# Kernel optimization log

Measured on AMD Instinct MI355X. Metric: run time of the kernel, lower is better.

Reference implementation:

```python
import jax, jax.numpy as jnp
import numpy as np


def setup_inputs() -> dict:
    key = jax.random.key(0)
    k1, k2, k3 = jax.random.split(key, 3)
    B, S, N = 32, 128, 256
    input_real = jax.random.normal(k1, (B, S, N), dtype=jnp.float32)
    input_imag = jax.random.normal(k2, (B, S, N), dtype=jnp.float32)
    weight = jax.random.uniform(k3, (B, S), dtype=jnp.float32)
    return {"input_real": input_real, "input_imag": input_imag, "weight": weight}


def reference(input_real, input_imag, weight):
    # Weighted mixture of rank-1 density matrices over the sequence dim S.
    # output_real[b,n,m] = sum_s w[b,s] * (r[b,s,n]*r[b,s,m] + i[b,s,n]*i[b,s,m])
    # output_imag[b,n,m] = sum_s w[b,s] * (i[b,s,n]*r[b,s,m] - r[b,s,n]*i[b,s,m])
    # Fused: pre-scale one factor by the weight, then a single contraction over S
    # (never materializes the [B,S,N,N] intermediates of the torch code).
    wr = input_real * weight[:, :, None]  # [B,S,N]
    wi = input_imag * weight[:, :, None]  # [B,S,N]
    output_r = jnp.einsum('bsn,bsm->bnm', wr, input_real) + jnp.einsum('bsn,bsm->bnm', wi, input_imag)
    output_i = jnp.einsum('bsn,bsm->bnm', wi, input_real) - jnp.einsum('bsn,bsm->bnm', wr, input_imag)
    return (output_r, output_i)
```

## Files before the change

kernel.cpp:

```cpp
#include <hip/hip_runtime.h>
#include <hip/hip_fp16.h>


constexpr int B = 32, S = 128, N = 256;

typedef _Float16 f16x8 __attribute__((ext_vector_type(8)));
typedef float    f32x4 __attribute__((ext_vector_type(4)));

union F16x8 { f16x8 v; __half2 h2[4]; };

#define MFMA16(a, bv, c) __builtin_amdgcn_mfma_f32_16x16x32_f16((a), (bv), (c), 0, 0, 0)

#define LBAR() {                                                             \
        __builtin_amdgcn_sched_barrier(0);                                   \
        asm volatile("s_waitcnt lgkmcnt(0)" ::: "memory");                   \
        __builtin_amdgcn_s_barrier();                                        \
        __builtin_amdgcn_sched_barrier(0); }

__global__ __launch_bounds__(512, 2) void ComplexMixture_71313636983193_kernel(
    const float* __restrict__ R, const float* __restrict__ I,
    const float* __restrict__ W, float* __restrict__ Or, float* __restrict__ Oi)
{
    __shared__ alignas(16) _Float16 T[6][64][128];

    const int pb   = blockIdx.x;
    const int lbid = (pb & 7) * 32 + (pb >> 3);
    const int b   = lbid >> 3;
    const int rem = lbid & 7;
    const int ti  = rem >> 1;
    const int uu  = rem & 1;
    const int tj1 = uu * 2, tj2 = uu * 2 + 1;

    const int t  = threadIdx.x;
    const int wv = t >> 6, lane = t & 63;

    const int nquad = t & 15;
    const int octet = (t >> 4) & 15;
    const int arr   = t >> 8;
    const int s0    = octet * 8;

    const size_t bb = (size_t)b * S * N;
    const float* base  = (arr ? I : R) + bb + nquad * 4;
    const float* srcA  = base + ti  * 64;
    const float* srcB1 = base + tj1 * 64;
    const float* srcB2 = base + tj2 * 64;
    const float* Wb = W + b * S;

    float4 fA[8], fB1[8];
    #pragma unroll
    for (int s = 0; s < 8; ++s)
        fA[s] = *(const float4*)&srcA[(size_t)(s0 + s) * N];
    #pragma unroll
    for (int s = 0; s < 8; ++s)
        fB1[s] = *(const float4*)&srcB1[(size_t)(s0 + s) * N];

    float w8[8];
    {
        const float4 a0 = *(const float4*)&Wb[s0];
        const float4 a1 = *(const float4*)&Wb[s0 + 4];
        w8[0]=a0.x; w8[1]=a0.y; w8[2]=a0.z; w8[3]=a0.w;
        w8[4]=a1.x; w8[5]=a1.y; w8[6]=a1.z; w8[7]=a1.w;
    }

    #pragma unroll
    for (int j = 0; j < 4; ++j) {
        const int n    = nquad * 4 + j;
        const int slot = octet ^ ((n >> 1) & 7);
        F16x8 fa, fb;
        #pragma unroll
        for (int k = 0; k < 4; ++k) {
            fa.h2[k] = __floats2half2_rn(((const float*)&fA[2*k])[j]   * w8[2*k],
                                         ((const float*)&fA[2*k+1])[j] * w8[2*k+1]);
            fb.h2[k] = __floats2half2_rn(((const float*)&fB1[2*k])[j],
                                         ((const float*)&fB1[2*k+1])[j]);
        }
        *(f16x8*)&T[arr][n][slot * 8]     = fa.v;
        *(f16x8*)&T[2 + arr][n][slot * 8] = fb.v;
    }

    float4 fB2[8];
    #pragma unroll
    for (int s = 0; s < 8; ++s)
        fB2[s] = *(const float4*)&srcB2[(size_t)(s0 + s) * N];

    LBAR();

    const int wn = (wv & 3) * 16;
    const int wm = (wv >> 2) * 32;
    const int fr16 = lane & 15, kb = lane >> 4;
    const int ra  = wn + fr16;          const int sa  = (ra  >> 1) & 7;
    const int rb0 = wm + fr16;          const int sb0 = (rb0 >> 1) & 7;
    const int rb1 = wm + 16 + fr16;     const int sb1 = (rb1 >> 1) & 7;

    f16x8 awr, awi;

#define LOAD_A(ks) { const int ca = (((ks) * 4 + kb) ^ sa) * 8;              \
        awr = *(const f16x8*)&T[0][ra][ca];                                  \
        awi = *(const f16x8*)&T[1][ra][ca]; }
#define STEP_B(TB, ks, ms, aR, aA, aB) { const int K = (ks) * 4 + kb;        \
        const int rb = (ms) ? rb1 : rb0;                                     \
        const int cb = (K ^ ((ms) ? sb1 : sb0)) * 8;                         \
        const f16x8 br = *(const f16x8*)&T[TB][rb][cb];                      \
        const f16x8 bi = *(const f16x8*)&T[(TB) + 1][rb][cb];                \
        aR[ms] = MFMA16(awr, br, aR[ms]);                                    \
        aR[ms] = MFMA16(awi, bi, aR[ms]);                                    \
        aA[ms] = MFMA16(awi, br, aA[ms]);                                    \
        aB[ms] = MFMA16(awr, bi, aB[ms]); }

    const int n0 = ti * 64;
    const int nn = n0 + wn + kb * 4;

#define STORE_MS(TJ, ms, aR, aA, aB) {                                       \
        const int mm = (TJ) * 64 + wm + (ms) * 16 + fr16;                    \
        _Pragma("unroll")                                                    \
        for (int r = 0; r < 4; ++r) {                                        \
            const size_t o = ((size_t)b * N + nn + r) * N + mm;              \
            Or[o] = aR[ms][r];                                               \
            Oi[o] = aA[ms][r] - aB[ms][r];                                   \
        } }

#define B2CVT(j) {                                                           \
        const int n    = nquad * 4 + (j);                                    \
        const int slot = octet ^ ((n >> 1) & 7);                             \
        F16x8 fb;                                                            \
        _Pragma("unroll")                                                    \
        for (int k = 0; k < 4; ++k)                                          \
            fb.h2[k] = __floats2half2_rn(((const float*)&fB2[2*k])[(j)],     \
                                         ((const float*)&fB2[2*k+1])[(j)]);  \
        *(f16x8*)&T[4 + arr][n][slot * 8] = fb.v; }

    f32x4 a1R[2] = {}, a1A[2] = {}, a1B[2] = {};
    __builtin_amdgcn_s_setprio(1);
    LOAD_A(0); STEP_B(2, 0, 0, a1R, a1A, a1B); STEP_B(2, 0, 1, a1R, a1A, a1B);
    LOAD_A(1); STEP_B(2, 1, 0, a1R, a1A, a1B); STEP_B(2, 1, 1, a1R, a1A, a1B);
    LOAD_A(2); STEP_B(2, 2, 0, a1R, a1A, a1B); STEP_B(2, 2, 1, a1R, a1A, a1B);
    LOAD_A(3); STEP_B(2, 3, 0, a1R, a1A, a1B); STEP_B(2, 3, 1, a1R, a1A, a1B);
    __builtin_amdgcn_s_setprio(0);

    STORE_MS(tj1, 0, a1R, a1A, a1B);
    B2CVT(0); B2CVT(1);
    STORE_MS(tj1, 1, a1R, a1A, a1B);
    B2CVT(2); B2CVT(3);

    LBAR();

    f32x4 a2R[2] = {}, a2A[2] = {}, a2B[2] = {};
    __builtin_amdgcn_s_setprio(1);
    LOAD_A(0); STEP_B(4, 0, 0, a2R, a2A, a2B); STEP_B(4, 0, 1, a2R, a2A, a2B);
    LOAD_A(1); STEP_B(4, 1, 0, a2R, a2A, a2B); STEP_B(4, 1, 1, a2R, a2A, a2B);
    LOAD_A(2); STEP_B(4, 2, 0, a2R, a2A, a2B); STEP_B(4, 2, 1, a2R, a2A, a2B);
    LOAD_A(3); STEP_B(4, 3, 0, a2R, a2A, a2B);
    __builtin_amdgcn_s_setprio(0);
    STORE_MS(tj2, 0, a2R, a2A, a2B);
    __builtin_amdgcn_s_setprio(1);
    STEP_B(4, 3, 1, a2R, a2A, a2B);
    __builtin_amdgcn_s_setprio(0);
    STORE_MS(tj2, 1, a2R, a2A, a2B);
}

extern "C" void kernel_launch(void* const* d_in, const int* in_sizes, int n_in,
                              void* d_out, int out_size, void* d_ws, size_t ws_size,
                              hipStream_t stream) {
    const float* R = (const float*)d_in[0];
    const float* I = (const float*)d_in[1];
    const float* W = (const float*)d_in[2];
    float* Or = (float*)d_out;
    float* Oi = (float*)d_out + (size_t)B * N * N;

    ComplexMixture_71313636983193_kernel<<<dim3(256), dim3(512), 0, stream>>>(
        R, I, W, Or, Oi);
}
```

Measured before the change: 12.73 us.

## Warp-specialize: half the waves compute tile 1 while others stage tile 2, use 32x32 MFMA

Switches from 16x16x32 MFMA tiles to 32x32x16 MFMA so each wave owns a 32x32 output tile. Instead of all 8 waves computing both output tiles in turn, waves 0-3 compute the first tile while waves 4-7 load and convert the second B tile into LDS. Waves 4-7 then compute the second tile while waves 0-3 store the first. This overlaps global loads and conversion with MFMA work, at the cost of each wave doing all compute for its tile and splitting the load work unevenly.

```diff
diff --git a/kernel.cpp b/kernel.cpp
--- a/kernel.cpp
+++ b/kernel.cpp
@@ -4,12 +4,12 @@
 
 constexpr int B = 32, S = 128, N = 256;
 
-typedef _Float16 f16x8 __attribute__((ext_vector_type(8)));
-typedef float    f32x4 __attribute__((ext_vector_type(4)));
+typedef _Float16 f16x8  __attribute__((ext_vector_type(8)));
+typedef float    f32x16 __attribute__((ext_vector_type(16)));
 
 union F16x8 { f16x8 v; __half2 h2[4]; };
 
-#define MFMA16(a, bv, c) __builtin_amdgcn_mfma_f32_16x16x32_f16((a), (bv), (c), 0, 0, 0)
+#define MFMA32(a, bv, c) __builtin_amdgcn_mfma_f32_32x32x16_f16((a), (bv), (c), 0, 0, 0)
 
 #define LBAR() {                                                             \
         __builtin_amdgcn_sched_barrier(0);                                   \
@@ -43,7 +43,6 @@
     const float* base  = (arr ? I : R) + bb + nquad * 4;
     const float* srcA  = base + ti  * 64;
     const float* srcB1 = base + tj1 * 64;
-    const float* srcB2 = base + tj2 * 64;
     const float* Wb = W + b * S;
 
     float4 fA[8], fB1[8];
@@ -78,84 +77,84 @@
         *(f16x8*)&T[2 + arr][n][slot * 8] = fb.v;
     }
 
-    float4 fB2[8];
-    #pragma unroll
-    for (int s = 0; s < 8; ++s)
-        fB2[s] = *(const float4*)&srcB2[(size_t)(s0 + s) * N];
+    float4 fB2R[8], fB2I[8];
+    if (wv >= 4) {
+        const float* sR = R + bb + tj2 * 64 + nquad * 4;
+        const float* sI = I + bb + tj2 * 64 + nquad * 4;
+        #pragma unroll
+        for (int s = 0; s < 8; ++s)
+            fB2R[s] = *(const float4*)&sR[(size_t)(s0 + s) * N];
+        #pragma unroll
+        for (int s = 0; s < 8; ++s)
+            fB2I[s] = *(const float4*)&sI[(size_t)(s0 + s) * N];
+    }
 
     LBAR();
 
-    const int wn = (wv & 3) * 16;
-    const int wm = (wv >> 2) * 32;
-    const int fr16 = lane & 15, kb = lane >> 4;
-    const int ra  = wn + fr16;          const int sa  = (ra  >> 1) & 7;
-    const int rb0 = wm + fr16;          const int sb0 = (rb0 >> 1) & 7;
-    const int rb1 = wm + 16 + fr16;     const int sb1 = (rb1 >> 1) & 7;
+    const int sn = (wv >> 1) & 1;
+    const int sm = wv & 1;
+    const int l31 = lane & 31, hi = lane >> 5;
+    const int rowA = sn * 32 + l31;    const int sgA = (rowA >> 1) & 7;
+    const int rowB = sm * 32 + l31;    const int sgB = (rowB >> 1) & 7;
 
-    f16x8 awr, awi;
+    f32x16 dR = {0,0,0,0,0,0,0,0,0,0,0,0,0,0,0,0};
+    f32x16 dA = {0,0,0,0,0,0,0,0,0,0,0,0,0,0,0,0};
+    f32x16 dB = {0,0,0,0,0,0,0,0,0,0,0,0,0,0,0,0};
 
-#define LOAD_A(ks) { const int ca = (((ks) * 4 + kb) ^ sa) * 8;              \
-        awr = *(const f16x8*)&T[0][ra][ca];                                  \
-        awi = *(const f16x8*)&T[1][ra][ca]; }
-#define STEP_B(TB, ks, ms, aR, aA, aB) { const int K = (ks) * 4 + kb;        \
-        const int rb = (ms) ? rb1 : rb0;                                     \
-        const int cb = (K ^ ((ms) ? sb1 : sb0)) * 8;                         \
-        const f16x8 br = *(const f16x8*)&T[TB][rb][cb];                      \
-        const f16x8 bi = *(const f16x8*)&T[(TB) + 1][rb][cb];                \
-        aR[ms] = MFMA16(awr, br, aR[ms]);                                    \
-        aR[ms] = MFMA16(awi, bi, aR[ms]);                                    \
-        aA[ms] = MFMA16(awi, br, aA[ms]);                                    \
-        aB[ms] = MFMA16(awr, bi, aB[ms]); }
+#define FRAG_STEP(TB, ks) {                                                  \
+        const int ca = ((2 * (ks) + hi) ^ sgA) * 8;                          \
+        const int cb = ((2 * (ks) + hi) ^ sgB) * 8;                          \
+        const f16x8 ar = *(const f16x8*)&T[0][rowA][ca];                     \
+        const f16x8 ai = *(const f16x8*)&T[1][rowA][ca];                     \
+        const f16x8 br = *(const f16x8*)&T[TB][rowB][cb];                    \
+        const f16x8 bi = *(const f16x8*)&T[(TB) + 1][rowB][cb];              \
+        dR = MFMA32(ar, br, dR); dR = MFMA32(ai, bi, dR);                    \
+        dA = MFMA32(ai, br, dA); dB = MFMA32(ar, bi, dB); }
 
-    const int n0 = ti * 64;
-    const int nn = n0 + wn + kb * 4;
-
-#define STORE_MS(TJ, ms, aR, aA, aB) {                                       \
-        const int mm = (TJ) * 64 + wm + (ms) * 16 + fr16;                    \
+#define STORE_TILE(TJ) {                                                     \
+        const int mm = (TJ) * 64 + sm * 32 + l31;                            \
         _Pragma("unroll")                                                    \
-        for (int r = 0; r < 4; ++r) {                                        \
-            const size_t o = ((size_t)b * N + nn + r) * N + mm;              \
-            Or[o] = aR[ms][r];                                               \
-            Oi[o] = aA[ms][r] - aB[ms][r];                                   \
+        for (int r = 0; r < 16; ++r) {                                       \
+            const int nn = ti * 64 + sn * 32 + (r & 3) + 8 * (r >> 2) + 4 * hi; \
+            const size_t o = ((size_t)b * N + nn) * N + mm;                  \
+            Or[o] = dR[r];                                                   \
+            Oi[o] = dA[r] - dB[r];                                           \
         } }
 
-#define B2CVT(j) {                                                           \
-        const int n    = nquad * 4 + (j);                                    \
-        const int slot = octet ^ ((n >> 1) & 7);                             \
-        F16x8 fb;                                                            \
-        _Pragma("unroll")                                                    \
-        for (int k = 0; k < 4; ++k)                                          \
-            fb.h2[k] = __floats2half2_rn(((const float*)&fB2[2*k])[(j)],     \
-                                         ((const float*)&fB2[2*k+1])[(j)]);  \
-        *(f16x8*)&T[4 + arr][n][slot * 8] = fb.v; }
-
-    f32x4 a1R[2] = {}, a1A[2] = {}, a1B[2] = {};
-    __builtin_amdgcn_s_setprio(1);
-    LOAD_A(0); STEP_B(2, 0, 0, a1R, a1A, a1B); STEP_B(2, 0, 1, a1R, a1A, a1B);
-    LOAD_A(1); STEP_B(2, 1, 0, a1R, a1A, a1B); STEP_B(2, 1, 1, a1R, a1A, a1B);
-    LOAD_A(2); STEP_B(2, 2, 0, a1R, a1A, a1B); STEP_B(2, 2, 1, a1R, a1A, a1B);
-    LOAD_A(3); STEP_B(2, 3, 0, a1R, a1A, a1B); STEP_B(2, 3, 1, a1R, a1A, a1B);
-    __builtin_amdgcn_s_setprio(0);
-
-    STORE_MS(tj1, 0, a1R, a1A, a1B);
-    B2CVT(0); B2CVT(1);
-    STORE_MS(tj1, 1, a1R, a1A, a1B);
-    B2CVT(2); B2CVT(3);
+    if (wv < 4) {
+        __builtin_amdgcn_s_setprio(1);
+        FRAG_STEP(2, 0); FRAG_STEP(2, 1); FRAG_STEP(2, 2); FRAG_STEP(2, 3);
+        FRAG_STEP(2, 4); FRAG_STEP(2, 5); FRAG_STEP(2, 6); FRAG_STEP(2, 7);
+        __builtin_amdgcn_s_setprio(0);
+    } else {
+        #pragma unroll
+        for (int j = 0; j < 4; ++j) {
+            const int n    = nquad * 4 + j;
+            const int slot = octet ^ ((n >> 1) & 7);
+            F16x8 fr, fi;
+            #pragma unroll
+            for (int k = 0; k < 4; ++k) {
+                fr.h2[k] = __floats2half2_rn(((const float*)&fB2R[2*k])[j],
+                                             ((const float*)&fB2R[2*k+1])[j]);
+                fi.h2[k] = __floats2half2_rn(((const float*)&fB2I[2*k])[j],
+                                             ((const float*)&fB2I[2*k+1])[j]);
+            }
+            *(f16x8*)&T[4][n][slot * 8] = fr.v;
+            *(f16x8*)&T[5][n][slot * 8] = fi.v;
+        }
+    }
 
     LBAR();
 
-    f32x4 a2R[2] = {}, a2A[2] = {}, a2B[2] = {};
-    __builtin_amdgcn_s_setprio(1);
-    LOAD_A(0); STEP_B(4, 0, 0, a2R, a2A, a2B); STEP_B(4, 0, 1, a2R, a2A, a2B);
-    LOAD_A(1); STEP_B(4, 1, 0, a2R, a2A, a2B); STEP_B(4, 1, 1, a2R, a2A, a2B);
-    LOAD_A(2); STEP_B(4, 2, 0, a2R, a2A, a2B); STEP_B(4, 2, 1, a2R, a2A, a2B);
-    LOAD_A(3); STEP_B(4, 3, 0, a2R, a2A, a2B);
-    __builtin_amdgcn_s_setprio(0);
-    STORE_MS(tj2, 0, a2R, a2A, a2B);
-    __builtin_amdgcn_s_setprio(1);
-    STEP_B(4, 3, 1, a2R, a2A, a2B);
-    __builtin_amdgcn_s_setprio(0);
-    STORE_MS(tj2, 1, a2R, a2A, a2B);
+    if (wv < 4) {
+        STORE_TILE(tj1);
+    } else {
+        __builtin_amdgcn_s_setprio(1);
+        FRAG_STEP(4, 0); FRAG_STEP(4, 1); FRAG_STEP(4, 2); FRAG_STEP(4, 3);
+        FRAG_STEP(4, 4); FRAG_STEP(4, 5); FRAG_STEP(4, 6); FRAG_STEP(4, 7);
+        __builtin_amdgcn_s_setprio(0);
+        STORE_TILE(tj2);
+    }
 }
 
 extern "C" void kernel_launch(void* const* d_in, const int* in_sizes, int n_in,
```

New measurement: 13.28 us. 1.04x slower.
